# Performance work log

Hardware: AMD Instinct MI355X
Metric: run time of the kernel (lower is better)

## Reference

```python
import jax, jax.numpy as jnp
import numpy as np
from jax import lax

B, T, C_IN, HID, K, HORIZON = 64, 1024, 256, 512, 3, 12
OUT_DIM = HORIZON * 3


def causal_conv(x, w, b, dilation):
    # x: (B, C_in, T), w: (C_out, C_in, K) -> left-padded causal conv == conv+Chomp1d
    pad = (K - 1) * dilation
    y = lax.conv_general_dilated(x, w, window_strides=(1,), padding=[(pad, 0)],
                                 rhs_dilation=(dilation,),
                                 dimension_numbers=('NCH', 'OIH', 'NCH'))
    return y + b[None, :, None]


def setup_inputs() -> dict:
    key = jax.random.key(0)
    ks = jax.random.split(key, 16)
    N = B * T
    x = jax.random.normal(ks[0], (N, C_IN), jnp.float32)
    edge_index = jax.random.randint(ks[1], (2, N), 0, N, dtype=jnp.int64)
    idx = jnp.arange(N, dtype=jnp.int64)
    batch = idx // T          # graph id per node
    node_time = idx % T       # local time per node
    s1 = 1.0 / np.sqrt(C_IN * K)
    s2 = 1.0 / np.sqrt(HID * K)
    sd = 1.0 / np.sqrt(C_IN)
    sf = 1.0 / np.sqrt(HID)
    return {
        'x': x, 'edge_index': edge_index, 'batch': batch, 'node_time': node_time,
        # TemporalBlock 0 (in=C_IN, out=HID, dilation=1)
        'conv1_w0': jax.random.uniform(ks[2], (HID, C_IN, K), jnp.float32, -s1, s1),
        'conv1_b0': jax.random.uniform(ks[3], (HID,), jnp.float32, -s1, s1),
        'conv2_w0': jax.random.uniform(ks[4], (HID, HID, K), jnp.float32, -s2, s2),
        'conv2_b0': jax.random.uniform(ks[5], (HID,), jnp.float32, -s2, s2),
        'down_w0': jax.random.uniform(ks[6], (HID, C_IN, 1), jnp.float32, -sd, sd),
        'down_b0': jax.random.uniform(ks[7], (HID,), jnp.float32, -sd, sd),
        # TemporalBlock 1 (in=HID, out=HID, dilation=2, no downsample)
        'conv1_w1': jax.random.uniform(ks[8], (HID, HID, K), jnp.float32, -s2, s2),
        'conv1_b1': jax.random.uniform(ks[9], (HID,), jnp.float32, -s2, s2),
        'conv2_w1': jax.random.uniform(ks[10], (HID, HID, K), jnp.float32, -s2, s2),
        'conv2_b1': jax.random.uniform(ks[11], (HID,), jnp.float32, -s2, s2),
        # fc
        'fc_w': jax.random.uniform(ks[12], (OUT_DIM, HID), jnp.float32, -sf, sf),
        'fc_b': jax.random.uniform(ks[13], (OUT_DIM,), jnp.float32, -sf, sf),
    }


def reference(x, edge_index, batch, node_time,
              conv1_w0, conv1_b0, conv2_w0, conv2_b0, down_w0, down_b0,
              conv1_w1, conv1_b1, conv2_w1, conv2_b1, fc_w, fc_b):
    # vectorized scatter replacing the per-node Python loop
    x_seq = jnp.zeros((B, T, C_IN), x.dtype).at[batch, node_time].set(x)
    h = x_seq.transpose(0, 2, 1)  # (B, C_IN, T)
    # TemporalBlock 0 (dropout inactive in eval)
    out = jax.nn.relu(causal_conv(h, conv1_w0, conv1_b0, 1))
    out = jax.nn.relu(causal_conv(out, conv2_w0, conv2_b0, 1))
    res = jnp.einsum('bct,oc->bot', h, down_w0[:, :, 0]) + down_b0[None, :, None]
    h = jax.nn.relu(out + res)
    # TemporalBlock 1
    out = jax.nn.relu(causal_conv(h, conv1_w1, conv1_b1, 2))
    out = jax.nn.relu(causal_conv(out, conv2_w1, conv2_b1, 2))
    h = jax.nn.relu(out + h)
    # last timestep -> fc
    return h[:, :, -1] @ fc_w.T + fc_b
```

## Files before the change

### kernel.cpp

```cpp
#include <hip/hip_runtime.h>


__device__ __forceinline__ float relu(float v) { return fmaxf(v, 0.f); }
__device__ __forceinline__ float4 relu4(float4 v) {
  v.x = fmaxf(v.x, 0.f); v.y = fmaxf(v.y, 0.f);
  v.z = fmaxf(v.z, 0.f); v.w = fmaxf(v.w, 0.f);
  return v;
}
__device__ __forceinline__ float4 add4(float4 a, float4 b) {
  a.x += b.x; a.y += b.y; a.z += b.z; a.w += b.w;
  return a;
}
__device__ __forceinline__ float4 addc4(float4 a, float c) {
  a.x += c; a.y += c; a.z += c; a.w += c;
  return a;
}
#define F4(q) (*(const float4*)(q))

__global__ __launch_bounds__(256) void kA(const float* __restrict__ x,
                                          const float* __restrict__ w1_0,
                                          const float* __restrict__ wd0,
                                          float* __restrict__ P0,
                                          float* __restrict__ PD) {
  __shared__ float smem[14288];
  const int tid = threadIdx.x, lane = tid & 63, wv = tid >> 6;
  if (blockIdx.x < 256) {
    const int ocp = blockIdx.x >> 3, ks = blockIdx.x & 7, oc0 = ocp * 16;
    float* Als = smem;
    float* Bls = smem + 768;
    float acc[4][11];
#pragma unroll
    for (int i = 0; i < 4; ++i)
#pragma unroll
      for (int t = 0; t < 11; ++t) acc[i][t] = 0.f;
    for (int ch = 0; ch < 2; ++ch) {
      const int c0 = ks * 32 + ch * 16;
      if (ch) __syncthreads();
      for (int idx = tid; idx < 768; idx += 256) {
        int i = idx / 48, r = idx % 48, c = r / 3, kk = r % 3;
        Als[(c * 3 + kk) * 16 + i] = w1_0[(oc0 + i) * 768 + (c0 + c) * 3 + kk];
      }
      for (int idx = tid; idx < 13312; idx += 256) {
        int c = idx & 15, b = (idx >> 4) & 63, u = idx >> 10;
        Bls[(c * 13 + u) * 65 + b] = x[(b * 1024 + 1011 + u) * 256 + c0 + c];
      }
      __syncthreads();
      for (int c = 0; c < 16; ++c) {
        float bv[13];
#pragma unroll
        for (int u = 0; u < 13; ++u) bv[u] = Bls[(c * 13 + u) * 65 + lane];
        float av[3][4];
#pragma unroll
        for (int kk = 0; kk < 3; ++kk)
          *(float4*)av[kk] = F4(&Als[(c * 3 + kk) * 16 + wv * 4]);
#pragma unroll
        for (int i = 0; i < 4; ++i)
#pragma unroll
          for (int t = 0; t < 11; ++t)
#pragma unroll
            for (int kk = 0; kk < 3; ++kk)
              acc[i][t] += av[kk][i] * bv[t + kk];
      }
    }
#pragma unroll
    for (int i = 0; i < 4; ++i)
#pragma unroll
      for (int t = 0; t < 11; ++t)
        P0[((ks * 512 + oc0 + wv * 4 + i) * 11 + t) * 64 + lane] = acc[i][t];
  } else {
    const int q = blockIdx.x - 256;
    const int ocp = q >> 3, ks = q & 7, oc0 = ocp * 32;
    float* Ad = smem;
    float* Bd = smem + 512;
    float acc[8][5];
#pragma unroll
    for (int i = 0; i < 8; ++i)
#pragma unroll
      for (int t = 0; t < 5; ++t) acc[i][t] = 0.f;
    for (int ch = 0; ch < 2; ++ch) {
      const int c0 = ks * 32 + ch * 16;
      if (ch) __syncthreads();
      for (int idx = tid; idx < 512; idx += 256) {
        int i = idx & 31, c = idx >> 5;
        Ad[c * 32 + i] = wd0[(oc0 + i) * 256 + c0 + c];
      }
      for (int idx = tid; idx < 5120; idx += 256) {
        int c = idx & 15, b = (idx >> 4) & 63, u = idx >> 10;
        Bd[(c * 5 + u) * 65 + b] = x[(b * 1024 + 1015 + 2 * u) * 256 + c0 + c];
      }
      __syncthreads();
      for (int c = 0; c < 16; ++c) {
        float bv[5];
#pragma unroll
        for (int u = 0; u < 5; ++u) bv[u] = Bd[(c * 5 + u) * 65 + lane];
        float av[8];
        *(float4*)&av[0] = F4(&Ad[c * 32 + wv * 8]);
        *(float4*)&av[4] = F4(&Ad[c * 32 + wv * 8 + 4]);
#pragma unroll
        for (int i = 0; i < 8; ++i)
#pragma unroll
          for (int t = 0; t < 5; ++t) acc[i][t] += av[i] * bv[t];
      }
    }
#pragma unroll
    for (int i = 0; i < 8; ++i)
#pragma unroll
      for (int t = 0; t < 5; ++t)
        PD[((ks * 512 + oc0 + wv * 8 + i) * 5 + t) * 64 + lane] = acc[i][t];
  }
}

__global__ __launch_bounds__(256) void kB(const float* __restrict__ P0,
                                          const float* __restrict__ b1_0,
                                          const float* __restrict__ w2_0,
                                          float* __restrict__ P1) {
  __shared__ float smem[12800];
  const int tid = threadIdx.x, lane = tid & 63, wv = tid >> 6;
  const int ocp = blockIdx.x >> 4, ks = blockIdx.x & 15, oc0 = ocp * 32;
  float* Als = smem;
  float* Bls = smem + 1536;
  float acc[8][5];
#pragma unroll
  for (int i = 0; i < 8; ++i)
#pragma unroll
    for (int t = 0; t < 5; ++t) acc[i][t] = 0.f;
  for (int ch = 0; ch < 2; ++ch) {
    const int c0 = ks * 32 + ch * 16;
    if (ch) __syncthreads();
    for (int idx = tid; idx < 1536; idx += 256) {
      int i = idx / 48, r = idx % 48, c = r / 3, kk = r % 3;
      Als[(c * 3 + kk) * 32 + i] = w2_0[(oc0 + i) * 1536 + (c0 + c) * 3 + kk];
    }
    for (int idx = tid; idx < 2816; idx += 256) {
      int c = idx / 176, r = idx % 176, u = r / 16, b4 = (r & 15) * 4;
      int cc = c0 + c;
      float4 s = {0.f, 0.f, 0.f, 0.f};
#pragma unroll
      for (int p = 0; p < 8; ++p)
        s = add4(s, F4(&P0[((p * 512 + cc) * 11 + u) * 64 + b4]));
      *(float4*)&Bls[(c * 11 + u) * 64 + b4] = relu4(addc4(s, b1_0[cc]));
    }
    __syncthreads();
    for (int c = 0; c < 16; ++c) {
      float bv[11];
#pragma unroll
      for (int u = 0; u < 11; ++u) bv[u] = Bls[(c * 11 + u) * 64 + lane];
      float av[3][8];
#pragma unroll
      for (int kk = 0; kk < 3; ++kk) {
        *(float4*)&av[kk][0] = F4(&Als[(c * 3 + kk) * 32 + wv * 8]);
        *(float4*)&av[kk][4] = F4(&Als[(c * 3 + kk) * 32 + wv * 8 + 4]);
      }
#pragma unroll
      for (int i = 0; i < 8; ++i)
#pragma unroll
        for (int t = 0; t < 5; ++t)
#pragma unroll
          for (int kk = 0; kk < 3; ++kk)
            acc[i][t] += av[kk][i] * bv[2 * t + kk];
    }
  }
#pragma unroll
  for (int i = 0; i < 8; ++i)
#pragma unroll
    for (int t = 0; t < 5; ++t)
      P1[((ks * 512 + oc0 + wv * 8 + i) * 5 + t) * 64 + lane] = acc[i][t];
}

__global__ __launch_bounds__(256) void kC(const float* __restrict__ P1,
                                          const float* __restrict__ b2_0,
                                          const float* __restrict__ PD,
                                          const float* __restrict__ bd0,
                                          const float* __restrict__ w1_1,
                                          float* __restrict__ P2,
                                          float* __restrict__ H0f) {
  __shared__ float smem[6656];
  const int tid = threadIdx.x, lane = tid & 63, wv = tid >> 6;
  const int ocp = blockIdx.x >> 4, ks = blockIdx.x & 15, oc0 = ocp * 32;
  float* Als = smem;
  float* Bls = smem + 1536;
  float acc[8][3];
#pragma unroll
  for (int i = 0; i < 8; ++i)
#pragma unroll
    for (int t = 0; t < 3; ++t) acc[i][t] = 0.f;
  for (int ch = 0; ch < 2; ++ch) {
    const int c0 = ks * 32 + ch * 16;
    if (ch) __syncthreads();
    for (int idx = tid; idx < 1536; idx += 256) {
      int i = idx / 48, r = idx % 48, c = r / 3, kk = r % 3;
      Als[(c * 3 + kk) * 32 + i] = w1_1[(oc0 + i) * 1536 + (c0 + c) * 3 + kk];
    }
    for (int idx = tid; idx < 1280; idx += 256) {
      int c = idx / 80, r = idx % 80, u = r / 16, b4 = (r & 15) * 4;
      int cc = c0 + c;
      float4 s = {0.f, 0.f, 0.f, 0.f};
#pragma unroll
      for (int p = 0; p < 16; ++p)
        s = add4(s, F4(&P1[((p * 512 + cc) * 5 + u) * 64 + b4]));
      s = relu4(addc4(s, b2_0[cc]));
      float4 d = {0.f, 0.f, 0.f, 0.f};
#pragma unroll
      for (int p = 0; p < 8; ++p)
        d = add4(d, F4(&PD[((p * 512 + cc) * 5 + u) * 64 + b4]));
      s = relu4(addc4(add4(s, d), bd0[cc]));
      *(float4*)&Bls[(c * 5 + u) * 64 + b4] = s;
      if (ocp == 0 && u == 4) *(float4*)&H0f[cc * 64 + b4] = s;
    }
    __syncthreads();
    for (int c = 0; c < 16; ++c) {
      float bv[5];
#pragma unroll
      for (int u = 0; u < 5; ++u) bv[u] = Bls[(c * 5 + u) * 64 + lane];
      float av[3][8];
#pragma unroll
      for (int kk = 0; kk < 3; ++kk) {
        *(float4*)&av[kk][0] = F4(&Als[(c * 3 + kk) * 32 + wv * 8]);
        *(float4*)&av[kk][4] = F4(&Als[(c * 3 + kk) * 32 + wv * 8 + 4]);
      }
#pragma unroll
      for (int i = 0; i < 8; ++i)
#pragma unroll
        for (int t = 0; t < 3; ++t)
#pragma unroll
          for (int kk = 0; kk < 3; ++kk)
            acc[i][t] += av[kk][i] * bv[t + kk];
    }
  }
#pragma unroll
  for (int i = 0; i < 8; ++i)
#pragma unroll
    for (int t = 0; t < 3; ++t)
      P2[((ks * 512 + oc0 + wv * 8 + i) * 3 + t) * 64 + lane] = acc[i][t];
}

__global__ __launch_bounds__(256) void kD(const float* __restrict__ P2,
                                          const float* __restrict__ b1_1,
                                          const float* __restrict__ w2_1,
                                          float* __restrict__ P3) {
  __shared__ float smem[18432];
  const int tid = threadIdx.x, lane = tid & 63, wv = tid >> 6;
  const int ocp = blockIdx.x >> 3, ks = blockIdx.x & 7, oc0 = ocp * 32;
  const int c0 = ks * 64;
  float* Als = smem;
  float* Bls = smem + 6144;
  float acc[8];
#pragma unroll
  for (int i = 0; i < 8; ++i) acc[i] = 0.f;
  for (int idx = tid; idx < 6144; idx += 256) {
    int i = idx / 192, r = idx % 192, c = r / 3, kk = r % 3;
    Als[(c * 3 + kk) * 32 + i] = w2_1[(oc0 + i) * 1536 + (c0 + c) * 3 + kk];
  }
  for (int idx = tid; idx < 3072; idx += 256) {
    int c = idx / 48, r = idx % 48, u = r / 16, b4 = (r & 15) * 4;
    int cc = c0 + c;
    float4 s = {0.f, 0.f, 0.f, 0.f};
#pragma unroll
    for (int p = 0; p < 16; ++p)
      s = add4(s, F4(&P2[((p * 512 + cc) * 3 + u) * 64 + b4]));
    *(float4*)&Bls[(c * 3 + u) * 64 + b4] = relu4(addc4(s, b1_1[cc]));
  }
  __syncthreads();
  for (int c = 0; c < 64; ++c) {
    float bv[3];
#pragma unroll
    for (int u = 0; u < 3; ++u) bv[u] = Bls[(c * 3 + u) * 64 + lane];
    float av[3][8];
#pragma unroll
    for (int kk = 0; kk < 3; ++kk) {
      *(float4*)&av[kk][0] = F4(&Als[(c * 3 + kk) * 32 + wv * 8]);
      *(float4*)&av[kk][4] = F4(&Als[(c * 3 + kk) * 32 + wv * 8 + 4]);
    }
#pragma unroll
    for (int i = 0; i < 8; ++i)
#pragma unroll
      for (int kk = 0; kk < 3; ++kk) acc[i] += av[kk][i] * bv[kk];
  }
#pragma unroll
  for (int i = 0; i < 8; ++i)
    P3[(ks * 512 + oc0 + wv * 8 + i) * 64 + lane] = acc[i];
}

__global__ __launch_bounds__(256) void kE(const float* __restrict__ P3,
                                          const float* __restrict__ b2_1,
                                          const float* __restrict__ H0f,
                                          const float* __restrict__ fcw,
                                          const float* __restrict__ fcb,
                                          float* __restrict__ out) {
  const int j = blockIdx.x, tid = threadIdx.x;
  const int lane = tid & 63, wv = tid >> 6;
  __shared__ float red[4][64];
  float partial = (wv == 0) ? fcb[j] : 0.f;
  for (int o = wv * 128; o < wv * 128 + 128; ++o) {
    float s = 0.f;
#pragma unroll
    for (int p = 0; p < 8; ++p) s += P3[(p * 512 + o) * 64 + lane];
    float h1 = relu(relu(s + b2_1[o]) + H0f[o * 64 + lane]);
    partial += fcw[j * 512 + o] * h1;
  }
  red[wv][lane] = partial;
  __syncthreads();
  if (wv == 0)
    out[lane * 36 + j] =
        red[0][lane] + red[1][lane] + red[2][lane] + red[3][lane];
}

extern "C" void kernel_launch(void* const* d_in, const int* in_sizes, int n_in,
                              void* d_out, int out_size, void* d_ws, size_t ws_size,
                              hipStream_t stream) {
  const float* x    = (const float*)d_in[0];
  const float* w1_0 = (const float*)d_in[4];
  const float* b1_0 = (const float*)d_in[5];
  const float* w2_0 = (const float*)d_in[6];
  const float* b2_0 = (const float*)d_in[7];
  const float* wd0  = (const float*)d_in[8];
  const float* bd0  = (const float*)d_in[9];
  const float* w1_1 = (const float*)d_in[10];
  const float* b1_1 = (const float*)d_in[11];
  const float* w2_1 = (const float*)d_in[12];
  const float* b2_1 = (const float*)d_in[13];
  const float* fcw  = (const float*)d_in[14];
  const float* fcb  = (const float*)d_in[15];
  float* out = (float*)d_out;

  float* P0  = (float*)d_ws;
  float* PD  = P0 + 2883584;
  float* P1  = PD + 1310720;
  float* P2  = P1 + 2621440;
  float* P3  = P2 + 1572864;
  float* H0f = P3 + 262144;

  kA<<<384, 256, 0, stream>>>(x, w1_0, wd0, P0, PD);
  kB<<<256, 256, 0, stream>>>(P0, b1_0, w2_0, P1);
  kC<<<256, 256, 0, stream>>>(P1, b2_0, PD, bd0, w1_1, P2, H0f);
  kD<<<128, 256, 0, stream>>>(P2, b1_1, w2_1, P3);
  kE<<<36, 256, 0, stream>>>(P3, b2_1, H0f, fcw, fcb, out);
}
```

Baseline: 125.4 us.

## Halve split-K factors across stages and pre-reduce downsample partials in kB

Cuts the split-K partition count in kA, kB and kC by half. kC and kD now compute 64 output channels per block instead of 32, so each block does more reuse of the loaded activations and fewer partial sums have to be written and re-reduced. The downsample partial reduction moves into extra work at the tail of kB, writing a pre-summed PDs buffer that kC reads. The cost is far fewer blocks (64-192) on a large GPU, so occupancy drops and each block runs longer, plus more registers per thread in kC and kD.

```diff
diff --git a/kernel.cpp b/kernel.cpp
--- a/kernel.cpp
+++ b/kernel.cpp
@@ -24,8 +24,8 @@
                                           float* __restrict__ PD) {
   __shared__ float smem[14288];
   const int tid = threadIdx.x, lane = tid & 63, wv = tid >> 6;
-  if (blockIdx.x < 256) {
-    const int ocp = blockIdx.x >> 3, ks = blockIdx.x & 7, oc0 = ocp * 16;
+  if (blockIdx.x < 128) {
+    const int ocp = blockIdx.x >> 2, ks = blockIdx.x & 3, oc0 = ocp * 16;
     float* Als = smem;
     float* Bls = smem + 768;
     float acc[4][11];
@@ -33,8 +33,8 @@
     for (int i = 0; i < 4; ++i)
 #pragma unroll
       for (int t = 0; t < 11; ++t) acc[i][t] = 0.f;
-    for (int ch = 0; ch < 2; ++ch) {
-      const int c0 = ks * 32 + ch * 16;
+    for (int ch = 0; ch < 4; ++ch) {
+      const int c0 = ks * 64 + ch * 16;
       if (ch) __syncthreads();
       for (int idx = tid; idx < 768; idx += 256) {
         int i = idx / 48, r = idx % 48, c = r / 3, kk = r % 3;
@@ -68,8 +68,8 @@
       for (int t = 0; t < 11; ++t)
         P0[((ks * 512 + oc0 + wv * 4 + i) * 11 + t) * 64 + lane] = acc[i][t];
   } else {
-    const int q = blockIdx.x - 256;
-    const int ocp = q >> 3, ks = q & 7, oc0 = ocp * 32;
+    const int q = blockIdx.x - 128;
+    const int ocp = q >> 2, ks = q & 3, oc0 = ocp * 32;
     float* Ad = smem;
     float* Bd = smem + 512;
     float acc[8][5];
@@ -77,8 +77,8 @@
     for (int i = 0; i < 8; ++i)
 #pragma unroll
       for (int t = 0; t < 5; ++t) acc[i][t] = 0.f;
-    for (int ch = 0; ch < 2; ++ch) {
-      const int c0 = ks * 32 + ch * 16;
+    for (int ch = 0; ch < 4; ++ch) {
+      const int c0 = ks * 64 + ch * 16;
       if (ch) __syncthreads();
       for (int idx = tid; idx < 512; idx += 256) {
         int i = idx & 31, c = idx >> 5;
@@ -113,10 +113,12 @@
 __global__ __launch_bounds__(256) void kB(const float* __restrict__ P0,
                                           const float* __restrict__ b1_0,
                                           const float* __restrict__ w2_0,
-                                          float* __restrict__ P1) {
+                                          const float* __restrict__ PD,
+                                          float* __restrict__ P1,
+                                          float* __restrict__ PDs) {
   __shared__ float smem[12800];
   const int tid = threadIdx.x, lane = tid & 63, wv = tid >> 6;
-  const int ocp = blockIdx.x >> 4, ks = blockIdx.x & 15, oc0 = ocp * 32;
+  const int ocp = blockIdx.x >> 3, ks = blockIdx.x & 7, oc0 = ocp * 32;
   float* Als = smem;
   float* Bls = smem + 1536;
   float acc[8][5];
@@ -124,8 +126,8 @@
   for (int i = 0; i < 8; ++i)
 #pragma unroll
     for (int t = 0; t < 5; ++t) acc[i][t] = 0.f;
-  for (int ch = 0; ch < 2; ++ch) {
-    const int c0 = ks * 32 + ch * 16;
+  for (int ch = 0; ch < 4; ++ch) {
+    const int c0 = ks * 64 + ch * 16;
     if (ch) __syncthreads();
     for (int idx = tid; idx < 1536; idx += 256) {
       int i = idx / 48, r = idx % 48, c = r / 3, kk = r % 3;
@@ -136,7 +138,7 @@
       int cc = c0 + c;
       float4 s = {0.f, 0.f, 0.f, 0.f};
 #pragma unroll
-      for (int p = 0; p < 8; ++p)
+      for (int p = 0; p < 4; ++p)
         s = add4(s, F4(&P0[((p * 512 + cc) * 11 + u) * 64 + b4]));
       *(float4*)&Bls[(c * 11 + u) * 64 + b4] = relu4(addc4(s, b1_0[cc]));
     }
@@ -165,45 +167,49 @@
 #pragma unroll
     for (int t = 0; t < 5; ++t)
       P1[((ks * 512 + oc0 + wv * 8 + i) * 5 + t) * 64 + lane] = acc[i][t];
+  for (int idx = blockIdx.x * 256 + tid; idx < 40960; idx += 128 * 256) {
+    int cc = idx / 80, r = idx % 80, u = r / 16, b4 = (r & 15) * 4;
+    float4 s = {0.f, 0.f, 0.f, 0.f};
+#pragma unroll
+    for (int p = 0; p < 4; ++p)
+      s = add4(s, F4(&PD[((p * 512 + cc) * 5 + u) * 64 + b4]));
+    *(float4*)&PDs[(cc * 5 + u) * 64 + b4] = s;
+  }
 }
 
 __global__ __launch_bounds__(256) void kC(const float* __restrict__ P1,
                                           const float* __restrict__ b2_0,
-                                          const float* __restrict__ PD,
+                                          const float* __restrict__ PDs,
                                           const float* __restrict__ bd0,
                                           const float* __restrict__ w1_1,
                                           float* __restrict__ P2,
                                           float* __restrict__ H0f) {
-  __shared__ float smem[6656];
+  __shared__ float smem[8192];
   const int tid = threadIdx.x, lane = tid & 63, wv = tid >> 6;
-  const int ocp = blockIdx.x >> 4, ks = blockIdx.x & 15, oc0 = ocp * 32;
+  const int ocp = blockIdx.x >> 3, ks = blockIdx.x & 7, oc0 = ocp * 64;
   float* Als = smem;
-  float* Bls = smem + 1536;
-  float acc[8][3];
-#pragma unroll
-  for (int i = 0; i < 8; ++i)
+  float* Bls = smem + 3072;
+  float acc[16][3];
+#pragma unroll
+  for (int i = 0; i < 16; ++i)
 #pragma unroll
     for (int t = 0; t < 3; ++t) acc[i][t] = 0.f;
-  for (int ch = 0; ch < 2; ++ch) {
-    const int c0 = ks * 32 + ch * 16;
+  for (int ch = 0; ch < 4; ++ch) {
+    const int c0 = ks * 64 + ch * 16;
     if (ch) __syncthreads();
-    for (int idx = tid; idx < 1536; idx += 256) {
+    for (int idx = tid; idx < 3072; idx += 256) {
       int i = idx / 48, r = idx % 48, c = r / 3, kk = r % 3;
-      Als[(c * 3 + kk) * 32 + i] = w1_1[(oc0 + i) * 1536 + (c0 + c) * 3 + kk];
+      Als[(c * 3 + kk) * 64 + i] = w1_1[(oc0 + i) * 1536 + (c0 + c) * 3 + kk];
     }
     for (int idx = tid; idx < 1280; idx += 256) {
       int c = idx / 80, r = idx % 80, u = r / 16, b4 = (r & 15) * 4;
       int cc = c0 + c;
       float4 s = {0.f, 0.f, 0.f, 0.f};
 #pragma unroll
-      for (int p = 0; p < 16; ++p)
+      for (int p = 0; p < 8; ++p)
         s = add4(s, F4(&P1[((p * 512 + cc) * 5 + u) * 64 + b4]));
       s = relu4(addc4(s, b2_0[cc]));
-      float4 d = {0.f, 0.f, 0.f, 0.f};
-#pragma unroll
-      for (int p = 0; p < 8; ++p)
-        d = add4(d, F4(&PD[((p * 512 + cc) * 5 + u) * 64 + b4]));
-      s = relu4(addc4(add4(s, d), bd0[cc]));
+      s = relu4(addc4(add4(s, F4(&PDs[(cc * 5 + u) * 64 + b4])), bd0[cc]));
       *(float4*)&Bls[(c * 5 + u) * 64 + b4] = s;
       if (ocp == 0 && u == 4) *(float4*)&H0f[cc * 64 + b4] = s;
     }
@@ -212,14 +218,14 @@
       float bv[5];
 #pragma unroll
       for (int u = 0; u < 5; ++u) bv[u] = Bls[(c * 5 + u) * 64 + lane];
-      float av[3][8];
-#pragma unroll
-      for (int kk = 0; kk < 3; ++kk) {
-        *(float4*)&av[kk][0] = F4(&Als[(c * 3 + kk) * 32 + wv * 8]);
-        *(float4*)&av[kk][4] = F4(&Als[(c * 3 + kk) * 32 + wv * 8 + 4]);
-      }
-#pragma unroll
-      for (int i = 0; i < 8; ++i)
+      float av[3][16];
+#pragma unroll
+      for (int kk = 0; kk < 3; ++kk)
+#pragma unroll
+        for (int j = 0; j < 16; j += 4)
+          *(float4*)&av[kk][j] = F4(&Als[(c * 3 + kk) * 64 + wv * 16 + j]);
+#pragma unroll
+      for (int i = 0; i < 16; ++i)
 #pragma unroll
         for (int t = 0; t < 3; ++t)
 #pragma unroll
@@ -228,35 +234,35 @@
     }
   }
 #pragma unroll
-  for (int i = 0; i < 8; ++i)
+  for (int i = 0; i < 16; ++i)
 #pragma unroll
     for (int t = 0; t < 3; ++t)
-      P2[((ks * 512 + oc0 + wv * 8 + i) * 3 + t) * 64 + lane] = acc[i][t];
+      P2[((ks * 512 + oc0 + wv * 16 + i) * 3 + t) * 64 + lane] = acc[i][t];
 }
 
 __global__ __launch_bounds__(256) void kD(const float* __restrict__ P2,
                                           const float* __restrict__ b1_1,
                                           const float* __restrict__ w2_1,
                                           float* __restrict__ P3) {
-  __shared__ float smem[18432];
+  __shared__ float smem[24576];
   const int tid = threadIdx.x, lane = tid & 63, wv = tid >> 6;
-  const int ocp = blockIdx.x >> 3, ks = blockIdx.x & 7, oc0 = ocp * 32;
+  const int ocp = blockIdx.x >> 3, ks = blockIdx.x & 7, oc0 = ocp * 64;
   const int c0 = ks * 64;
   float* Als = smem;
-  float* Bls = smem + 6144;
-  float acc[8];
-#pragma unroll
-  for (int i = 0; i < 8; ++i) acc[i] = 0.f;
-  for (int idx = tid; idx < 6144; idx += 256) {
+  float* Bls = smem + 12288;
+  float acc[16];
+#pragma unroll
+  for (int i = 0; i < 16; ++i) acc[i] = 0.f;
+  for (int idx = tid; idx < 12288; idx += 256) {
     int i = idx / 192, r = idx % 192, c = r / 3, kk = r % 3;
-    Als[(c * 3 + kk) * 32 + i] = w2_1[(oc0 + i) * 1536 + (c0 + c) * 3 + kk];
+    Als[(c * 3 + kk) * 64 + i] = w2_1[(oc0 + i) * 1536 + (c0 + c) * 3 + kk];
   }
   for (int idx = tid; idx < 3072; idx += 256) {
     int c = idx / 48, r = idx % 48, u = r / 16, b4 = (r & 15) * 4;
     int cc = c0 + c;
     float4 s = {0.f, 0.f, 0.f, 0.f};
 #pragma unroll
-    for (int p = 0; p < 16; ++p)
+    for (int p = 0; p < 8; ++p)
       s = add4(s, F4(&P2[((p * 512 + cc) * 3 + u) * 64 + b4]));
     *(float4*)&Bls[(c * 3 + u) * 64 + b4] = relu4(addc4(s, b1_1[cc]));
   }
@@ -265,20 +271,20 @@
     float bv[3];
 #pragma unroll
     for (int u = 0; u < 3; ++u) bv[u] = Bls[(c * 3 + u) * 64 + lane];
-    float av[3][8];
-#pragma unroll
-    for (int kk = 0; kk < 3; ++kk) {
-      *(float4*)&av[kk][0] = F4(&Als[(c * 3 + kk) * 32 + wv * 8]);
-      *(float4*)&av[kk][4] = F4(&Als[(c * 3 + kk) * 32 + wv * 8 + 4]);
-    }
-#pragma unroll
-    for (int i = 0; i < 8; ++i)
+    float av[3][16];
+#pragma unroll
+    for (int kk = 0; kk < 3; ++kk)
+#pragma unroll
+      for (int j = 0; j < 16; j += 4)
+        *(float4*)&av[kk][j] = F4(&Als[(c * 3 + kk) * 64 + wv * 16 + j]);
+#pragma unroll
+    for (int i = 0; i < 16; ++i)
 #pragma unroll
       for (int kk = 0; kk < 3; ++kk) acc[i] += av[kk][i] * bv[kk];
   }
 #pragma unroll
-  for (int i = 0; i < 8; ++i)
-    P3[(ks * 512 + oc0 + wv * 8 + i) * 64 + lane] = acc[i];
+  for (int i = 0; i < 16; ++i)
+    P3[(ks * 512 + oc0 + wv * 16 + i) * 64 + lane] = acc[i];
 }
 
 __global__ __launch_bounds__(256) void kE(const float* __restrict__ P3,
@@ -324,15 +330,16 @@
   float* out = (float*)d_out;
 
   float* P0  = (float*)d_ws;
-  float* PD  = P0 + 2883584;
-  float* P1  = PD + 1310720;
-  float* P2  = P1 + 2621440;
-  float* P3  = P2 + 1572864;
+  float* PD  = P0 + 1441792;
+  float* PDs = PD + 655360;
+  float* P1  = PDs + 163840;
+  float* P2  = P1 + 1310720;
+  float* P3  = P2 + 786432;
   float* H0f = P3 + 262144;
 
-  kA<<<384, 256, 0, stream>>>(x, w1_0, wd0, P0, PD);
-  kB<<<256, 256, 0, stream>>>(P0, b1_0, w2_0, P1);
-  kC<<<256, 256, 0, stream>>>(P1, b2_0, PD, bd0, w1_1, P2, H0f);
-  kD<<<128, 256, 0, stream>>>(P2, b1_1, w2_1, P3);
+  kA<<<192, 256, 0, stream>>>(x, w1_0, wd0, P0, PD);
+  kB<<<128, 256, 0, stream>>>(P0, b1_0, w2_0, PD, P1, PDs);
+  kC<<<64, 256, 0, stream>>>(P1, b2_0, PDs, bd0, w1_1, P2, H0f);
+  kD<<<64, 256, 0, stream>>>(P2, b1_1, w2_1, P3);
   kE<<<36, 256, 0, stream>>>(P3, b2_1, H0f, fcw, fcb, out);
 }
```

Result: slower. 179.4 us (+43.0%).
